# Performance work log

Measured on AMD Instinct MI355X. Metric: run time of the kernel, lower is better.

Reference implementation:

```python
import jax, jax.numpy as jnp
import numpy as np

N_FEATURES = 1024
N_HEADS = 16
D_ATTN = 64


def setup_inputs() -> dict:
    key = jax.random.key(0)
    k_x, k_qkv, k_pw, k_pb = jax.random.split(key, 4)
    B, S = 2, 2048
    x = jax.random.normal(k_x, (B, S, N_FEATURES), dtype=jnp.float32)
    # torch nn.Linear weights are [out, in]; init scale ~ 1/sqrt(in)
    w_qkv = jax.random.normal(k_qkv, (3 * N_HEADS * D_ATTN, N_FEATURES), dtype=jnp.float32) / np.sqrt(N_FEATURES)
    w_proj = jax.random.normal(k_pw, (N_FEATURES, N_HEADS * D_ATTN), dtype=jnp.float32) / np.sqrt(N_HEADS * D_ATTN)
    b_proj = jax.random.normal(k_pb, (N_FEATURES,), dtype=jnp.float32) / np.sqrt(N_HEADS * D_ATTN)
    return {"x": x, "w_qkv": w_qkv, "w_proj": w_proj, "b_proj": b_proj}


def reference(x, w_qkv, w_proj, b_proj):
    B, S, F = x.shape
    H, D = N_HEADS, D_ATTN
    # fused QKV projection (bias=False): [B,S,3*H*D]
    qkv = jnp.einsum('bsf,of->bso', x, w_qkv)
    qkv = qkv.reshape(B, S, 3, H, D)
    q = jnp.transpose(qkv[:, :, 0], (0, 2, 1, 3))  # [B,H,S,D]
    k = jnp.transpose(qkv[:, :, 1], (0, 2, 1, 3))
    v = jnp.transpose(qkv[:, :, 2], (0, 2, 1, 3))
    scale = 1.0 / jnp.sqrt(jnp.asarray(D, dtype=x.dtype))
    scores = jnp.einsum('bhqd,bhkd->bhqk', q, k) * scale  # [B,H,S,S]
    attn = jax.nn.softmax(scores, axis=-1)
    out = jnp.einsum('bhqk,bhkd->bhqd', attn, v)  # [B,H,S,D]
    out = jnp.transpose(out, (0, 2, 1, 3)).reshape(B, S, H * D)
    # output projection (dropout is identity in eval mode)
    return jnp.einsum('bsm,fm->bsf', out, w_proj) + b_proj
```

## Files before the change

### kernel.cpp

```cpp
#include <hip/hip_runtime.h>
#include <hip/hip_bf16.h>
#include <math.h>

#define BATCH 2
#define SEQ 2048
#define NFEAT 1024
#define NHEAD 16
#define DHEAD 64
#define MROWS (BATCH * SEQ)
#define NQKV (3 * NHEAD * DHEAD)

typedef __attribute__((ext_vector_type(8))) short short8;
typedef __attribute__((ext_vector_type(4))) float floatx4;

#define CEXP 0.18033688f

__device__ __forceinline__ unsigned short f2bf(float f) {
    unsigned int u = __float_as_uint(f);
    u += 0x7fff + ((u >> 16) & 1);
    return (unsigned short)(u >> 16);
}

__device__ __forceinline__ float bf2f(unsigned short u) {
    return __uint_as_float((unsigned int)u << 16);
}

__device__ __forceinline__ float fast_exp2(float x) {
    return __builtin_amdgcn_exp2f(x);
}

__device__ __forceinline__ uint pack_bf16x2(float lo, float hi) {
    float2 t; t.x = lo; t.y = hi;
    __hip_bfloat162 h = __float22bfloat162_rn(t);
    union { __hip_bfloat162 h; uint u; } c; c.h = h;
    return c.u;
}

__device__ __forceinline__ void async16(const void* g, void* l) {
    __builtin_amdgcn_global_load_lds(
        (const __attribute__((address_space(1))) void*)g,
        (__attribute__((address_space(3))) void*)l, 16, 0, 0);
}

__global__ void cvt_swz(const float* __restrict__ x, const float* __restrict__ wq,
                        const float* __restrict__ wp,
                        ushort* __restrict__ xb, ushort* __restrict__ wqb,
                        ushort* __restrict__ wpb) {
    const int NX = MROWS * NFEAT / 4, NWQ = NQKV * NFEAT / 4, NWP = NFEAT * NFEAT / 4;
    int i = blockIdx.x * blockDim.x + threadIdx.x;
    if (i >= NX + NWQ + NWP) return;
    const float* src; ushort* dst; int idx4;
    if (i < NX)            { src = x;  dst = xb;  idx4 = i; }
    else if (i < NX + NWQ) { src = wq; dst = wqb; idx4 = i - NX; }
    else                   { src = wp; dst = wpb; idx4 = i - NX - NWQ; }
    float4 v = ((const float4*)src)[idx4];
    ushort4 o;
    o.x = f2bf(v.x); o.y = f2bf(v.y); o.z = f2bf(v.z); o.w = f2bf(v.w);
    const int e = idx4 * 4;
    const int k = e & (NFEAT - 1);
    const int row = e >> 10;
    const int kp = (k & ~31) | (((((k >> 3) & 3) ^ ((row >> 1) & 3))) << 3) | (k & 7);
    *(ushort4*)(dst + (size_t)row * NFEAT + kp) = o;
}

__global__ __launch_bounds__(256, 3)
void gemm_qkv(const ushort* __restrict__ A, const ushort* __restrict__ W,
              ushort* __restrict__ qb, ushort* __restrict__ kb, ushort* __restrict__ vtb) {
    __shared__ ushort smem[8192];
    ushort* As = smem;
    ushort* Bs = smem + 4096;
    const int tid = threadIdx.x;
    const int wave = tid >> 6, lane = tid & 63;
    const int m0 = blockIdx.y * 128, n0 = blockIdx.x * 128;
    const int wm = (wave >> 1) * 64, wn = (wave & 1) * 64;
    const int lr = lane & 15, lg = lane >> 4;
    const int kswz = (lg ^ ((lr >> 1) & 3)) * 8;

    floatx4 acc[4][4] = {};

    const int seg0 = tid, seg1 = tid + 256;
    const int row0 = seg0 >> 2, cb0 = (seg0 & 3) * 8;
    const int row1 = seg1 >> 2, cb1 = (seg1 & 3) * 8;

    for (int k0 = 0; k0 < NFEAT; k0 += 32) {
        async16(A + (size_t)(m0 + row0) * NFEAT + k0 + cb0, (void*)(As + seg0 * 8));
        async16(A + (size_t)(m0 + row1) * NFEAT + k0 + cb1, (void*)(As + seg1 * 8));
        async16(W + (size_t)(n0 + row0) * NFEAT + k0 + cb0, (void*)(Bs + seg0 * 8));
        async16(W + (size_t)(n0 + row1) * NFEAT + k0 + cb1, (void*)(Bs + seg1 * 8));
        __syncthreads();
        short8 a[4], b[4];
#pragma unroll
        for (int i = 0; i < 4; ++i)
            a[i] = *(const short8*)(As + (wm + i * 16 + lr) * 32 + kswz);
#pragma unroll
        for (int j = 0; j < 4; ++j)
            b[j] = *(const short8*)(Bs + (wn + j * 16 + lr) * 32 + kswz);
#pragma unroll
        for (int i = 0; i < 4; ++i)
#pragma unroll
            for (int j = 0; j < 4; ++j)
                acc[i][j] = __builtin_amdgcn_mfma_f32_16x16x32_bf16(a[i], b[j], acc[i][j], 0, 0, 0);
        __syncthreads();
    }

    const int t = n0 >> 10;
    const int bidx = m0 >> 11;
    if (t < 2) {
#pragma unroll
        for (int i = 0; i < 4; ++i)
#pragma unroll
            for (int j = 0; j < 4; ++j)
#pragma unroll
                for (int r = 0; r < 4; ++r) {
                    const int m = m0 + wm + i * 16 + lg * 4 + r;
                    const int n = n0 + wn + j * 16 + lr;
                    const int s = m & (SEQ - 1);
                    const int rem = n & 1023, h = rem >> 6, d = rem & 63;
                    if (t == 0) {
                        qb[((size_t)(bidx * NHEAD + h) * SEQ + s) * DHEAD + d] =
                            f2bf(acc[i][j][r] * CEXP);
                    } else {
                        const int dcol = ((((d >> 3) ^ (s & 7)) << 3)) | (d & 7);
                        kb[((size_t)(bidx * NHEAD + h) * SEQ + s) * DHEAD + dcol] =
                            f2bf(acc[i][j][r]);
                    }
                }
    } else {
#pragma unroll
        for (int hhalf = 0; hhalf < 2; ++hhalf) {
            if ((wm >> 6) == hhalf) {
#pragma unroll
                for (int i = 0; i < 4; ++i) {
                    const int chunk = i * 2 + (lg >> 1);
#pragma unroll
                    for (int j = 0; j < 4; ++j) {
                        const int n = wn + j * 16 + lr;
                        uint2 pk;
                        pk.x = pack_bf16x2(acc[i][j][0], acc[i][j][1]);
                        pk.y = pack_bf16x2(acc[i][j][2], acc[i][j][3]);
                        *(uint2*)(smem + n * 64 + ((chunk ^ (n & 7)) * 8) + (lg & 1) * 4) = pk;
                    }
                }
            }
            __syncthreads();
            const int s_base = (m0 & (SEQ - 1)) + hhalf * 64;
#pragma unroll
            for (int it = 0; it < 4; ++it) {
                const int n_r = (tid >> 3) + it * 32;
                const int p = tid & 7;
                short8 rowv = *(const short8*)(smem + n_r * 64 + p * 8);
                const int nglob = n0 + n_r;
                const int d = nglob & 63, hh = (nglob & 1023) >> 6;
                *(short8*)(vtb + ((size_t)(bidx * NHEAD + hh) * DHEAD + d) * SEQ + s_base + p * 8) = rowv;
            }
            __syncthreads();
        }
    }
}

__global__ __launch_bounds__(256, 2)
void gemm_proj(const ushort* __restrict__ A, const ushort* __restrict__ W,
               const float* __restrict__ bias, float* __restrict__ Cout) {
    __shared__ ushort As[128 * 32];
    __shared__ ushort Bs[64 * 32];
    const int tid = threadIdx.x;
    const int wave = tid >> 6, lane = tid & 63;
    const int m0 = blockIdx.y * 128, n0 = blockIdx.x * 64;
    const int wm = (wave >> 1) * 64, wn = (wave & 1) * 32;
    const int lr = lane & 15, lg = lane >> 4;
    const int kswz = (lg ^ ((lr >> 1) & 3)) * 8;

    floatx4 acc[4][2] = {};

    const int rowA = tid >> 2, cb = (tid & 3) * 8;

    for (int k0 = 0; k0 < NFEAT; k0 += 32) {
        async16(A + (size_t)(m0 + rowA) * NFEAT + k0 + cb, (void*)(As + tid * 8));
        async16(A + (size_t)(m0 + rowA + 64) * NFEAT + k0 + cb, (void*)(As + (tid + 256) * 8));
        async16(W + (size_t)(n0 + rowA) * NFEAT + k0 + cb, (void*)(Bs + tid * 8));
        __syncthreads();
        short8 a[4], b[2];
#pragma unroll
        for (int i = 0; i < 4; ++i)
            a[i] = *(const short8*)(As + (wm + i * 16 + lr) * 32 + kswz);
#pragma unroll
        for (int j = 0; j < 2; ++j)
            b[j] = *(const short8*)(Bs + (wn + j * 16 + lr) * 32 + kswz);
#pragma unroll
        for (int i = 0; i < 4; ++i)
#pragma unroll
            for (int j = 0; j < 2; ++j)
                acc[i][j] = __builtin_amdgcn_mfma_f32_16x16x32_bf16(a[i], b[j], acc[i][j], 0, 0, 0);
        __syncthreads();
    }

#pragma unroll
    for (int i = 0; i < 4; ++i)
#pragma unroll
        for (int j = 0; j < 2; ++j)
#pragma unroll
            for (int r = 0; r < 4; ++r) {
                const int m = m0 + wm + i * 16 + lg * 4 + r;
                const int n = n0 + wn + j * 16 + lr;
                Cout[(size_t)m * NFEAT + n] = acc[i][j][r] + bias[n];
            }
}

#define PSTRIDE 40
__global__ __launch_bounds__(256, 4)
void flash_attn(const ushort* __restrict__ qb, const ushort* __restrict__ kb,
                const ushort* __restrict__ vtb,
                ushort* __restrict__ op0, ushort* __restrict__ op1,
                float* __restrict__ lp0, float* __restrict__ lp1) {
    const int qt = blockIdx.x, ks = blockIdx.y, bh = blockIdx.z;
    const int tid = threadIdx.x, wave = tid >> 6, lane = tid & 63;
    const int lr = lane & 15, lg = lane >> 4;

    __shared__ ushort Ks[2][32 * 64];
    __shared__ ushort Vs[2][64 * 64];
    __shared__ ushort Ps_all[4][32 * PSTRIDE];
    ushort* Ps = Ps_all[wave];

    const ushort* Qb = qb + (size_t)bh * SEQ * DHEAD;
    const ushort* Kb = kb + (size_t)bh * SEQ * DHEAD;
    const ushort* Vt = vtb + (size_t)bh * DHEAD * SEQ;

    const int q0 = qt * 128 + wave * 32;
    const int kvbase = ks * (SEQ / 2);

    short8 qf[2][2];
#pragma unroll
    for (int j = 0; j < 2; ++j)
#pragma unroll
        for (int kk = 0; kk < 2; ++kk)
            qf[j][kk] = *(const short8*)(Qb + (size_t)(q0 + j * 16 + lr) * DHEAD + kk * 32 + lg * 8);

    const int krow = tid >> 3, kseg = (tid & 7) * 8;
    const size_t vrow = (size_t)(tid >> 3) * SEQ;
    const int vseg = (tid & 7) * 8;

#define STAGE_K(BUF, KV0) \
    async16(Kb + (size_t)((KV0) + krow) * DHEAD + kseg, (void*)(Ks[BUF] + tid * 8));
#define STAGE_V(BUF, KV0) \
    async16(Vt + vrow + (KV0) + vseg,            (void*)(Vs[BUF] + tid * 8)); \
    async16(Vt + 32 * SEQ + vrow + (KV0) + vseg, (void*)(Vs[BUF] + 2048 + tid * 8));

    STAGE_K(0, kvbase)
    STAGE_V(0, kvbase)

    floatx4 acc_o[2][4] = {};
    float l_lane[2] = {0.0f, 0.0f};
    const int sw = lr & 7;

#define FLASH_COMPUTE(KBUF, VB, KVH)                                                \
    {                                                                               \
        floatx4 st[2][2] = {};                                                      \
        _Pragma("unroll")                                                           \
        for (int kk = 0; kk < 2; ++kk)                                              \
            _Pragma("unroll")                                                       \
            for (int i = 0; i < 2; ++i) {                                           \
                short8 kf = *(const short8*)(Ks[KBUF] + (i * 16 + lr) * 64 +        \
                                             (((kk * 4 + lg) ^ sw) * 8));           \
                _Pragma("unroll")                                                   \
                for (int j = 0; j < 2; ++j)                                         \
                    st[i][j] = __builtin_amdgcn_mfma_f32_16x16x32_bf16(kf, qf[j][kk], st[i][j], 0, 0, 0); \
            }                                                                       \
        _Pragma("unroll")                                                           \
        for (int i = 0; i < 2; ++i)                                                 \
            _Pragma("unroll")                                                       \
            for (int j = 0; j < 2; ++j) {                                           \
                const float p0 = fast_exp2(st[i][j][0]);                            \
                const float p1 = fast_exp2(st[i][j][1]);                            \
                const float p2 = fast_exp2(st[i][j][2]);                            \
                const float p3 = fast_exp2(st[i][j][3]);                            \
                l_lane[j] += (p0 + p1) + (p2 + p3);                                 \
                uint2 pk;                                                           \
                pk.x = pack_bf16x2(p0, p1);                                         \
                pk.y = pack_bf16x2(p2, p3);                                         \
                *(uint2*)(Ps + (j * 16 + lr) * PSTRIDE + i * 16 + lg * 4) = pk;     \
            }                                                                       \
        {                                                                           \
            short8 vf[4];                                                           \
            _Pragma("unroll")                                                       \
            for (int j2 = 0; j2 < 4; ++j2)                                          \
                vf[j2] = *(const short8*)(Vs[VB] + (j2 * 16 + lr) * 64 +            \
                                          ((((KVH) * 4 + lg) ^ sw) * 8));           \
            _Pragma("unroll")                                                       \
            for (int i2 = 0; i2 < 2; ++i2) {                                        \
                short8 pf = *(const short8*)(Ps + (i2 * 16 + lr) * PSTRIDE + lg * 8); \
                _Pragma("unroll")                                                   \
                for (int j2 = 0; j2 < 4; ++j2)                                      \
                    acc_o[i2][j2] = __builtin_amdgcn_mfma_f32_16x16x32_bf16(pf, vf[j2], acc_o[i2][j2], 0, 0, 0); \
            }                                                                       \
        }                                                                           \
    }

    const int NT = (SEQ / 2) / 32;
    for (int t = 0; t < NT; t += 2) {
        const int vb = (t >> 1) & 1;
        __syncthreads();
        STAGE_K(1, kvbase + (t + 1) * 32)
        if (t + 2 < NT) { STAGE_V(1 - vb, kvbase + (t + 2) * 32) }
        FLASH_COMPUTE(0, vb, 0)
        __syncthreads();
        if (t + 2 < NT) { STAGE_K(0, kvbase + (t + 2) * 32) }
        FLASH_COMPUTE(1, vb, 1)
    }
#undef FLASH_COMPUTE
#undef STAGE_K
#undef STAGE_V

#pragma unroll
    for (int j = 0; j < 2; ++j) {
        l_lane[j] += __shfl_xor(l_lane[j], 16);
        l_lane[j] += __shfl_xor(l_lane[j], 32);
    }
    ushort* op = ks ? op1 : op0;
    float* lp = ks ? lp1 : lp0;
    if (lg == 0) {
#pragma unroll
        for (int j = 0; j < 2; ++j)
            lp[(size_t)bh * SEQ + q0 + j * 16 + lr] = l_lane[j];
    }

    const int b = bh >> 4, h = bh & 15;
#pragma unroll
    for (int i2 = 0; i2 < 2; ++i2) {
#pragma unroll
        for (int r = 0; r < 4; ++r) {
            const int srow = b * SEQ + q0 + i2 * 16 + lg * 4 + r;
#pragma unroll
            for (int j2 = 0; j2 < 4; ++j2) {
                const int d = j2 * 16 + lr;
                op[(size_t)srow * (NHEAD * DHEAD) + h * DHEAD + d] = f2bf(acc_o[i2][j2][r]);
            }
        }
    }
}

__global__ void combine(const ushort* __restrict__ o0, const ushort* __restrict__ o1,
                        const float* __restrict__ l0, const float* __restrict__ l1,
                        ushort* __restrict__ aout) {
    const int idx = blockIdx.x * 256 + threadIdx.x;
    const int srow = idx >> 7;
    const int k8 = (idx & 127) * 8;
    const int b = srow >> 11, s = srow & (SEQ - 1);
    const int h = k8 >> 6;
    const size_t lidx = (size_t)(b * NHEAD + h) * SEQ + s;
    const float inv = 1.0f / (l0[lidx] + l1[lidx]);
    short8 a = *(const short8*)(o0 + (size_t)srow * NFEAT + k8);
    short8 c = *(const short8*)(o1 + (size_t)srow * NFEAT + k8);
    uint2 lohi[2];
    uint pk[4];
#pragma unroll
    for (int e = 0; e < 4; ++e) {
        const float f0 = (bf2f((unsigned short)a[2 * e]) + bf2f((unsigned short)c[2 * e])) * inv;
        const float f1 = (bf2f((unsigned short)a[2 * e + 1]) + bf2f((unsigned short)c[2 * e + 1])) * inv;
        pk[e] = pack_bf16x2(f0, f1);
    }
    lohi[0].x = pk[0]; lohi[0].y = pk[1]; lohi[1].x = pk[2]; lohi[1].y = pk[3];
    const int cidx = (k8 >> 3) & 3, key = (srow >> 1) & 3;
    const int kp = (k8 & ~31) | ((cidx ^ key) * 8);
    *(uint2*)(aout + (size_t)srow * NFEAT + kp) = lohi[0];
    *(uint2*)(aout + (size_t)srow * NFEAT + kp + 4) = lohi[1];
}

extern "C" void kernel_launch(void* const* d_in, const int* in_sizes, int n_in,
                              void* d_out, int out_size, void* d_ws, size_t ws_size,
                              hipStream_t stream) {
    const float* x      = (const float*)d_in[0];
    const float* w_qkv  = (const float*)d_in[1];
    const float* w_proj = (const float*)d_in[2];
    const float* b_proj = (const float*)d_in[3];
    float* out = (float*)d_out;

    ushort* ws = (ushort*)d_ws;
    ushort* xb     = ws;
    ushort* wqkvb  = xb + (size_t)MROWS * NFEAT;
    ushort* wprojb = wqkvb + (size_t)NQKV * NFEAT;
    ushort* qb     = wprojb + (size_t)NFEAT * NFEAT;
    ushort* kb     = qb + (size_t)MROWS * NFEAT;
    ushort* vtb    = kb + (size_t)MROWS * NFEAT;
    ushort* aob    = vtb + (size_t)MROWS * NFEAT;

    ushort* op0 = aob;
    ushort* op1 = xb;
    float* lp0 = (float*)wqkvb;
    float* lp1 = lp0 + (size_t)BATCH * NHEAD * SEQ;
    ushort* acmb = kb;

    {
        const int total = (MROWS * NFEAT + NQKV * NFEAT + NFEAT * NFEAT) / 4;
        cvt_swz<<<(total + 255) / 256, 256, 0, stream>>>(x, w_qkv, w_proj, xb, wqkvb, wprojb);
    }

    {
        dim3 grid(NQKV / 128, MROWS / 128);
        gemm_qkv<<<grid, 256, 0, stream>>>(xb, wqkvb, qb, kb, vtb);
    }

    {
        dim3 grid(SEQ / 128, 2, BATCH * NHEAD);
        flash_attn<<<grid, 256, 0, stream>>>(qb, kb, vtb, op0, op1, lp0, lp1);
    }

    {
        const int total = MROWS * (NFEAT / 8);
        combine<<<total / 256, 256, 0, stream>>>(op0, op1, lp0, lp1, acmb);
    }

    {
        dim3 grid(NFEAT / 64, MROWS / 128);
        gemm_proj<<<grid, 256, 0, stream>>>(acmb, wprojb, b_proj, out);
    }
}
```

Baseline: 189.3 us.

## Fuse split-attention combine into projection GEMM and vectorize QKV epilogue stores

Removes the separate combine kernel by having the projection GEMM load both partial attention outputs and the row sums, normalize and pack to bf16 in registers, and write the swizzled A tile into LDS itself, with register prefetch of the next K slice. The QKV GEMM swaps MFMA operand order so each lane holds four consecutive output features and can emit packed 8-byte stores. The V transpose now writes directly with a swizzled sequence layout instead of going through LDS. The softmax scale is folded into the Q rows of the weight during conversion. This cuts a kernel launch and an intermediate buffer round trip, at the cost of extra ALU work and synchronous global loads inside the projection GEMM loop. The new V layout must match what the attention kernel expects.

```diff
diff --git a/kernel.cpp b/kernel.cpp
--- a/kernel.cpp
+++ b/kernel.cpp
@@ -47,15 +47,18 @@
                         ushort* __restrict__ xb, ushort* __restrict__ wqb,
                         ushort* __restrict__ wpb) {
     const int NX = MROWS * NFEAT / 4, NWQ = NQKV * NFEAT / 4, NWP = NFEAT * NFEAT / 4;
+    const int NWQ_Q = NFEAT * NFEAT / 4;
     int i = blockIdx.x * blockDim.x + threadIdx.x;
     if (i >= NX + NWQ + NWP) return;
     const float* src; ushort* dst; int idx4;
+    float sc = 1.0f;
     if (i < NX)            { src = x;  dst = xb;  idx4 = i; }
-    else if (i < NX + NWQ) { src = wq; dst = wqb; idx4 = i - NX; }
+    else if (i < NX + NWQ) { src = wq; dst = wqb; idx4 = i - NX;
+                             if (idx4 < NWQ_Q) sc = CEXP; }
     else                   { src = wp; dst = wpb; idx4 = i - NX - NWQ; }
     float4 v = ((const float4*)src)[idx4];
     ushort4 o;
-    o.x = f2bf(v.x); o.y = f2bf(v.y); o.z = f2bf(v.z); o.w = f2bf(v.w);
+    o.x = f2bf(v.x * sc); o.y = f2bf(v.y * sc); o.z = f2bf(v.z * sc); o.w = f2bf(v.w * sc);
     const int e = idx4 * 4;
     const int k = e & (NFEAT - 1);
     const int row = e >> 10;
@@ -66,15 +69,15 @@
 __global__ __launch_bounds__(256, 3)
 void gemm_qkv(const ushort* __restrict__ A, const ushort* __restrict__ W,
               ushort* __restrict__ qb, ushort* __restrict__ kb, ushort* __restrict__ vtb) {
-    __shared__ ushort smem[8192];
-    ushort* As = smem;
-    ushort* Bs = smem + 4096;
+    __shared__ ushort As[4096];
+    __shared__ ushort Bs[4096];
     const int tid = threadIdx.x;
     const int wave = tid >> 6, lane = tid & 63;
     const int m0 = blockIdx.y * 128, n0 = blockIdx.x * 128;
     const int wm = (wave >> 1) * 64, wn = (wave & 1) * 64;
     const int lr = lane & 15, lg = lane >> 4;
     const int kswz = (lg ^ ((lr >> 1) & 3)) * 8;
+    const bool qkmode = (n0 < 2048);
 
     floatx4 acc[4][4] = {};
 
@@ -88,78 +91,76 @@
         async16(W + (size_t)(n0 + row0) * NFEAT + k0 + cb0, (void*)(Bs + seg0 * 8));
         async16(W + (size_t)(n0 + row1) * NFEAT + k0 + cb1, (void*)(Bs + seg1 * 8));
         __syncthreads();
-        short8 a[4], b[4];
-#pragma unroll
-        for (int i = 0; i < 4; ++i)
-            a[i] = *(const short8*)(As + (wm + i * 16 + lr) * 32 + kswz);
-#pragma unroll
-        for (int j = 0; j < 4; ++j)
-            b[j] = *(const short8*)(Bs + (wn + j * 16 + lr) * 32 + kswz);
-#pragma unroll
-        for (int i = 0; i < 4; ++i)
-#pragma unroll
-            for (int j = 0; j < 4; ++j)
-                acc[i][j] = __builtin_amdgcn_mfma_f32_16x16x32_bf16(a[i], b[j], acc[i][j], 0, 0, 0);
-        __syncthreads();
-    }
-
-    const int t = n0 >> 10;
+        short8 fx[4], fw[4];
+#pragma unroll
+        for (int i = 0; i < 4; ++i) {
+            fx[i] = *(const short8*)(As + (wm + i * 16 + lr) * 32 + kswz);
+            fw[i] = *(const short8*)(Bs + (wn + i * 16 + lr) * 32 + kswz);
+        }
+        if (qkmode) {
+#pragma unroll
+            for (int i = 0; i < 4; ++i)
+#pragma unroll
+                for (int j = 0; j < 4; ++j)
+                    acc[i][j] = __builtin_amdgcn_mfma_f32_16x16x32_bf16(fw[i], fx[j], acc[i][j], 0, 0, 0);
+        } else {
+#pragma unroll
+            for (int i = 0; i < 4; ++i)
+#pragma unroll
+                for (int j = 0; j < 4; ++j)
+                    acc[i][j] = __builtin_amdgcn_mfma_f32_16x16x32_bf16(fx[i], fw[j], acc[i][j], 0, 0, 0);
+        }
+        __syncthreads();
+    }
+
     const int bidx = m0 >> 11;
-    if (t < 2) {
-#pragma unroll
-        for (int i = 0; i < 4; ++i)
-#pragma unroll
-            for (int j = 0; j < 4; ++j)
-#pragma unroll
-                for (int r = 0; r < 4; ++r) {
-                    const int m = m0 + wm + i * 16 + lg * 4 + r;
-                    const int n = n0 + wn + j * 16 + lr;
-                    const int s = m & (SEQ - 1);
-                    const int rem = n & 1023, h = rem >> 6, d = rem & 63;
-                    if (t == 0) {
-                        qb[((size_t)(bidx * NHEAD + h) * SEQ + s) * DHEAD + d] =
-                            f2bf(acc[i][j][r] * CEXP);
-                    } else {
-                        const int dcol = ((((d >> 3) ^ (s & 7)) << 3)) | (d & 7);
-                        kb[((size_t)(bidx * NHEAD + h) * SEQ + s) * DHEAD + dcol] =
-                            f2bf(acc[i][j][r]);
-                    }
-                }
-    } else {
-#pragma unroll
-        for (int hhalf = 0; hhalf < 2; ++hhalf) {
-            if ((wm >> 6) == hhalf) {
-#pragma unroll
-                for (int i = 0; i < 4; ++i) {
-                    const int chunk = i * 2 + (lg >> 1);
-#pragma unroll
-                    for (int j = 0; j < 4; ++j) {
-                        const int n = wn + j * 16 + lr;
-                        uint2 pk;
-                        pk.x = pack_bf16x2(acc[i][j][0], acc[i][j][1]);
-                        pk.y = pack_bf16x2(acc[i][j][2], acc[i][j][3]);
-                        *(uint2*)(smem + n * 64 + ((chunk ^ (n & 7)) * 8) + (lg & 1) * 4) = pk;
-                    }
+    if (qkmode) {
+        const bool isq = (n0 < 1024);
+#pragma unroll
+        for (int i = 0; i < 4; ++i) {
+#pragma unroll
+            for (int j = 0; j < 4; ++j) {
+                const int nbase = n0 + wn + i * 16 + lg * 4;
+                const int m = m0 + wm + j * 16 + lr;
+                const int s = m & (SEQ - 1);
+                const int rem = nbase & 1023;
+                const int h = rem >> 6, dbase = rem & 63;
+                uint2 pk;
+                pk.x = pack_bf16x2(acc[i][j][0], acc[i][j][1]);
+                pk.y = pack_bf16x2(acc[i][j][2], acc[i][j][3]);
+                if (isq) {
+                    *(uint2*)(qb + ((size_t)(bidx * NHEAD + h) * SEQ + s) * DHEAD + dbase) = pk;
+                } else {
+                    const int dcol = ((((dbase >> 3) ^ (s & 7)) << 3)) | (dbase & 7);
+                    *(uint2*)(kb + ((size_t)(bidx * NHEAD + h) * SEQ + s) * DHEAD + dcol) = pk;
                 }
             }
-            __syncthreads();
-            const int s_base = (m0 & (SEQ - 1)) + hhalf * 64;
-#pragma unroll
-            for (int it = 0; it < 4; ++it) {
-                const int n_r = (tid >> 3) + it * 32;
-                const int p = tid & 7;
-                short8 rowv = *(const short8*)(smem + n_r * 64 + p * 8);
-                const int nglob = n0 + n_r;
-                const int d = nglob & 63, hh = (nglob & 1023) >> 6;
-                *(short8*)(vtb + ((size_t)(bidx * NHEAD + hh) * DHEAD + d) * SEQ + s_base + p * 8) = rowv;
+        }
+    } else {
+#pragma unroll
+        for (int i = 0; i < 4; ++i) {
+#pragma unroll
+            for (int j = 0; j < 4; ++j) {
+                const int mbase = m0 + wm + i * 16 + lg * 4;
+                const int sbase = mbase & (SEQ - 1);
+                const int n = n0 + wn + j * 16 + lr;
+                const int rem = n & 1023;
+                const int h = rem >> 6, d = rem & 63;
+                const int chunk = ((sbase >> 3) & 7) ^ (d & 7);
+                const int scol = (sbase & ~63) | (chunk << 3) | (sbase & 7);
+                uint2 pk;
+                pk.x = pack_bf16x2(acc[i][j][0], acc[i][j][1]);
+                pk.y = pack_bf16x2(acc[i][j][2], acc[i][j][3]);
+                *(uint2*)(vtb + ((size_t)(bidx * NHEAD + h) * DHEAD + d) * SEQ + scol) = pk;
             }
-            __syncthreads();
         }
     }
 }
 
 __global__ __launch_bounds__(256, 2)
-void gemm_proj(const ushort* __restrict__ A, const ushort* __restrict__ W,
+void gemm_proj(const ushort* __restrict__ op0, const ushort* __restrict__ op1,
+               const float* __restrict__ l0, const float* __restrict__ l1,
+               const ushort* __restrict__ W,
                const float* __restrict__ bias, float* __restrict__ Cout) {
     __shared__ ushort As[128 * 32];
     __shared__ ushort Bs[64 * 32];
@@ -170,40 +171,78 @@
     const int lr = lane & 15, lg = lane >> 4;
     const int kswz = (lg ^ ((lr >> 1) & 3)) * 8;
 
-    floatx4 acc[4][2] = {};
+    floatx4 acc[2][4] = {};
 
     const int rowA = tid >> 2, cb = (tid & 3) * 8;
+    const int mA0 = m0 + rowA, mA1 = mA0 + 64;
+    const int sA0 = mA0 & (SEQ - 1), sA1 = mA1 & (SEQ - 1);
+    const int bb = mA0 >> 11;
+    const int slot0 = (((cb >> 3) ^ ((mA0 >> 1) & 3)) << 3);
+    const int slot1 = (((cb >> 3) ^ ((mA1 >> 1) & 3)) << 3);
+    const size_t aoff0 = (size_t)mA0 * NFEAT + cb;
+    const size_t aoff1 = (size_t)mA1 * NFEAT + cb;
+    const size_t lb0 = (size_t)(bb * NHEAD) * SEQ + sA0;
+    const size_t lb1 = (size_t)(bb * NHEAD) * SEQ + sA1;
+
+    short8 a00 = *(const short8*)(op0 + aoff0);
+    short8 a01 = *(const short8*)(op1 + aoff0);
+    short8 a10 = *(const short8*)(op0 + aoff1);
+    short8 a11 = *(const short8*)(op1 + aoff1);
 
     for (int k0 = 0; k0 < NFEAT; k0 += 32) {
-        async16(A + (size_t)(m0 + rowA) * NFEAT + k0 + cb, (void*)(As + tid * 8));
-        async16(A + (size_t)(m0 + rowA + 64) * NFEAT + k0 + cb, (void*)(As + (tid + 256) * 8));
+        const int h = k0 >> 6;
+        const float inv0 = 1.0f / (l0[lb0 + (size_t)h * SEQ] + l1[lb0 + (size_t)h * SEQ]);
+        const float inv1 = 1.0f / (l0[lb1 + (size_t)h * SEQ] + l1[lb1 + (size_t)h * SEQ]);
+        union { uint u[4]; short8 s; } c0, c1;
+#pragma unroll
+        for (int e = 0; e < 4; ++e) {
+            c0.u[e] = pack_bf16x2(
+                (bf2f((unsigned short)a00[2 * e])     + bf2f((unsigned short)a01[2 * e]))     * inv0,
+                (bf2f((unsigned short)a00[2 * e + 1]) + bf2f((unsigned short)a01[2 * e + 1])) * inv0);
+            c1.u[e] = pack_bf16x2(
+                (bf2f((unsigned short)a10[2 * e])     + bf2f((unsigned short)a11[2 * e]))     * inv1,
+                (bf2f((unsigned short)a10[2 * e + 1]) + bf2f((unsigned short)a11[2 * e + 1])) * inv1);
+        }
+        *(short8*)(As + rowA * 32 + slot0) = c0.s;
+        *(short8*)(As + (rowA + 64) * 32 + slot1) = c1.s;
         async16(W + (size_t)(n0 + rowA) * NFEAT + k0 + cb, (void*)(Bs + tid * 8));
-        __syncthreads();
-        short8 a[4], b[2];
-#pragma unroll
-        for (int i = 0; i < 4; ++i)
-            a[i] = *(const short8*)(As + (wm + i * 16 + lr) * 32 + kswz);
-#pragma unroll
-        for (int j = 0; j < 2; ++j)
-            b[j] = *(const short8*)(Bs + (wn + j * 16 + lr) * 32 + kswz);
-#pragma unroll
-        for (int i = 0; i < 4; ++i)
-#pragma unroll
-            for (int j = 0; j < 2; ++j)
-                acc[i][j] = __builtin_amdgcn_mfma_f32_16x16x32_bf16(a[i], b[j], acc[i][j], 0, 0, 0);
-        __syncthreads();
-    }
-
-#pragma unroll
-    for (int i = 0; i < 4; ++i)
-#pragma unroll
-        for (int j = 0; j < 2; ++j)
-#pragma unroll
-            for (int r = 0; r < 4; ++r) {
-                const int m = m0 + wm + i * 16 + lg * 4 + r;
-                const int n = n0 + wn + j * 16 + lr;
-                Cout[(size_t)m * NFEAT + n] = acc[i][j][r] + bias[n];
-            }
+        if (k0 + 32 < NFEAT) {
+            a00 = *(const short8*)(op0 + aoff0 + k0 + 32);
+            a01 = *(const short8*)(op1 + aoff0 + k0 + 32);
+            a10 = *(const short8*)(op0 + aoff1 + k0 + 32);
+            a11 = *(const short8*)(op1 + aoff1 + k0 + 32);
+        }
+        __syncthreads();
+        short8 fw[2], fa[4];
+#pragma unroll
+        for (int i = 0; i < 2; ++i)
+            fw[i] = *(const short8*)(Bs + (wn + i * 16 + lr) * 32 + kswz);
+#pragma unroll
+        for (int j = 0; j < 4; ++j)
+            fa[j] = *(const short8*)(As + (wm + j * 16 + lr) * 32 + kswz);
+#pragma unroll
+        for (int i = 0; i < 2; ++i)
+#pragma unroll
+            for (int j = 0; j < 4; ++j)
+                acc[i][j] = __builtin_amdgcn_mfma_f32_16x16x32_bf16(fw[i], fa[j], acc[i][j], 0, 0, 0);
+        __syncthreads();
+    }
+
+#pragma unroll
+    for (int i = 0; i < 2; ++i) {
+        const int nbase = n0 + wn + i * 16 + lg * 4;
+        const float4 bv = *(const float4*)(bias + nbase);
+#pragma unroll
+        for (int j = 0; j < 4; ++j) {
+            const int m = m0 + wm + j * 16 + lr;
+            float4 o;
+            o.x = acc[i][j][0] + bv.x;
+            o.y = acc[i][j][1] + bv.y;
+            o.z = acc[i][j][2] + bv.z;
+            o.w = acc[i][j][3] + bv.w;
+            *(float4*)(Cout + (size_t)m * NFEAT + nbase) = o;
+        }
+    }
 }
 
 #define PSTRIDE 40
@@ -338,33 +377,6 @@
     }
 }
 
-__global__ void combine(const ushort* __restrict__ o0, const ushort* __restrict__ o1,
-                        const float* __restrict__ l0, const float* __restrict__ l1,
-                        ushort* __restrict__ aout) {
-    const int idx = blockIdx.x * 256 + threadIdx.x;
-    const int srow = idx >> 7;
-    const int k8 = (idx & 127) * 8;
-    const int b = srow >> 11, s = srow & (SEQ - 1);
-    const int h = k8 >> 6;
-    const size_t lidx = (size_t)(b * NHEAD + h) * SEQ + s;
-    const float inv = 1.0f / (l0[lidx] + l1[lidx]);
-    short8 a = *(const short8*)(o0 + (size_t)srow * NFEAT + k8);
-    short8 c = *(const short8*)(o1 + (size_t)srow * NFEAT + k8);
-    uint2 lohi[2];
-    uint pk[4];
-#pragma unroll
-    for (int e = 0; e < 4; ++e) {
-        const float f0 = (bf2f((unsigned short)a[2 * e]) + bf2f((unsigned short)c[2 * e])) * inv;
-        const float f1 = (bf2f((unsigned short)a[2 * e + 1]) + bf2f((unsigned short)c[2 * e + 1])) * inv;
-        pk[e] = pack_bf16x2(f0, f1);
-    }
-    lohi[0].x = pk[0]; lohi[0].y = pk[1]; lohi[1].x = pk[2]; lohi[1].y = pk[3];
-    const int cidx = (k8 >> 3) & 3, key = (srow >> 1) & 3;
-    const int kp = (k8 & ~31) | ((cidx ^ key) * 8);
-    *(uint2*)(aout + (size_t)srow * NFEAT + kp) = lohi[0];
-    *(uint2*)(aout + (size_t)srow * NFEAT + kp + 4) = lohi[1];
-}
-
 extern "C" void kernel_launch(void* const* d_in, const int* in_sizes, int n_in,
                               void* d_out, int out_size, void* d_ws, size_t ws_size,
                               hipStream_t stream) {
@@ -387,7 +399,6 @@
     ushort* op1 = xb;
     float* lp0 = (float*)wqkvb;
     float* lp1 = lp0 + (size_t)BATCH * NHEAD * SEQ;
-    ushort* acmb = kb;
 
     {
         const int total = (MROWS * NFEAT + NQKV * NFEAT + NFEAT * NFEAT) / 4;
@@ -405,12 +416,7 @@
     }
 
     {
-        const int total = MROWS * (NFEAT / 8);
-        combine<<<total / 256, 256, 0, stream>>>(op0, op1, lp0, lp1, acmb);
-    }
-
-    {
         dim3 grid(NFEAT / 64, MROWS / 128);
-        gemm_proj<<<grid, 256, 0, stream>>>(acmb, wprojb, b_proj, out);
-    }
-}
+        gemm_proj<<<grid, 256, 0, stream>>>(op0, op1, lp0, lp1, wprojb, b_proj, out);
+    }
+}
```

Result: slower. 258.9 us (+36.8%).
